# Kernel tuning notes

Hardware: AMD Instinct MI355X
Metric: run time of the kernel (lower is better)

Reference implementation:

```python
import jax, jax.numpy as jnp
import numpy as np

N_NODES = 100000
N_EDGES = 1600000
D_IN = 128
D_OUT = 256


def setup_inputs() -> dict:
    key = jax.random.key(0)
    k1, k2, k3 = jax.random.split(key, 3)
    H = jax.random.normal(k1, (N_NODES, D_IN), dtype=jnp.float32)
    edge_index = jax.random.randint(k2, (2, N_EDGES), 0, N_NODES, dtype=jnp.int64)
    # kaiming_normal_ on (in, out): fan computed over dim 1 -> std = sqrt(2/out)
    W = jax.random.normal(k3, (D_IN, D_OUT), dtype=jnp.float32) * np.sqrt(2.0 / D_OUT)
    return {"H": H, "edge_index": edge_index, "W": W}


def reference(H, edge_index, W):
    src, dst = edge_index[0], edge_index[1]
    # gather source node features per edge, scatter-add into destination nodes
    msgs = H[src]  # [E, D_IN]
    new_H = jax.ops.segment_sum(msgs, dst, num_segments=H.shape[0])  # [N, D_IN]
    out = H + new_H
    out = out @ W  # [N, D_OUT]
    return jax.nn.relu(out)
```

## Files before the change

kernel.cpp:

```cpp
#include <hip/hip_runtime.h>

#define N_NODES 100000
#define N_EDGES 1600000
#define D_IN    128
#define D_OUT   256
#define NB_SCAN ((N_NODES + 255) / 256)
#define BLK_ROWS 64
#define N_TILES  ((N_NODES + BLK_ROWS - 1) / BLK_ROWS)
#define X_ROWS   (N_TILES * BLK_ROWS)

#define NBUCK      98
#define BCAP       20480
#define BIN_CHUNK  1024
#define BIN_BLOCKS ((N_EDGES + BIN_CHUNK - 1) / BIN_CHUNK)

#define GBLK_ROWS  32
#define G_TILES    ((N_NODES + GBLK_ROWS - 1) / GBLK_ROWS)

typedef __attribute__((ext_vector_type(8))) short short8v;
typedef __attribute__((ext_vector_type(4))) float f32x4;

__device__ __forceinline__ unsigned bf16_rn(float f) {
    unsigned u = __float_as_uint(f);
    return (u + 0x7FFFu + ((u >> 16) & 1u)) >> 16;
}
__device__ __forceinline__ unsigned pack2_bf16(float a, float b) {
    return bf16_rn(a) | (bf16_rn(b) << 16);
}

__global__ void detect_idx64_kernel(const int* __restrict__ edge32,
                                    int* __restrict__ flag) {
    if (threadIdx.x == 0 && blockIdx.x == 0) {
        int is64 = 1;
        for (int i = 1; i < 32; i += 2) {
            if (edge32[i] != 0) { is64 = 0; break; }
        }
        *flag = is64;
    }
}

__device__ __forceinline__ int load_dst(const void* edge_raw, int is64, int e) {
    if (is64) return (int)((const long long*)edge_raw)[(long long)N_EDGES + e];
    return ((const int*)edge_raw)[N_EDGES + e];
}
__device__ __forceinline__ int load_src(const void* edge_raw, int is64, int e) {
    if (is64) return (int)((const long long*)edge_raw)[e];
    return ((const int*)edge_raw)[e];
}

__global__ __launch_bounds__(256) void cvt_h_kernel(
        const float* __restrict__ H, unsigned* __restrict__ Hb) {
    int i = blockIdx.x * 256 + threadIdx.x;
    if (i >= N_NODES * (D_IN / 2)) return;
    const float2 h = ((const float2*)H)[i];
    Hb[i] = pack2_bf16(h.x, h.y);
}

__global__ __launch_bounds__(256) void pack_w_kernel(
        const float* __restrict__ W, unsigned short* __restrict__ Wp) {
    int t = blockIdx.x * 256 + threadIdx.x;
    if (t >= 64 * 64) return;
    const int f  = t >> 6;
    const int l  = t & 63;
    const int nb = f >> 2;
    const int ks = f & 3;
    const int col  = nb * 16 + (l & 15);
    const int krow = ks * 32 + (l >> 4) * 8;
    #pragma unroll
    for (int i = 0; i < 8; ++i)
        Wp[(size_t)t * 8 + i] = (unsigned short)bf16_rn(W[(krow + i) * D_OUT + col]);
}

__global__ __launch_bounds__(256) void bin_hist_kernel(
        const void* __restrict__ edge_raw, const int* __restrict__ flag,
        int* __restrict__ bucket_alloc, int* __restrict__ binned) {
    __shared__ int cnt[128];
    __shared__ int gbase[128];
    const int tid = threadIdx.x;
    if (tid < 128) cnt[tid] = 0;
    __syncthreads();
    const int is64 = *flag;
    const int base = blockIdx.x * BIN_CHUNK + tid;

#define EDGE_A(i)                                                             \
    int rec##i = 0, pb##i = -1;                                               \
    {                                                                         \
        const int idx = base + (i) * 256;                                     \
        if (idx < N_EDGES) {                                                  \
            const int s = load_src(edge_raw, is64, idx);                      \
            const int d = load_dst(edge_raw, is64, idx);                      \
            if ((unsigned)s < N_NODES && (unsigned)d < N_NODES) {             \
                const int b = d >> 10;                                        \
                const int pos = atomicAdd(&cnt[b], 1);                        \
                rec##i = s | ((d & 1023) << 17);                              \
                pb##i  = pos | (b << 12);                                     \
            }                                                                 \
        }                                                                     \
    }
    EDGE_A(0) EDGE_A(1) EDGE_A(2) EDGE_A(3)
#undef EDGE_A

    __syncthreads();
    if (tid < NBUCK) gbase[tid] = atomicAdd(&bucket_alloc[tid], cnt[tid]);
    __syncthreads();

#define EDGE_B(i)                                                             \
    if (pb##i >= 0) {                                                         \
        const int b = pb##i >> 12;                                            \
        const int p = gbase[b] + (pb##i & 4095);                              \
        if (p < BCAP) binned[b * BCAP + p] = rec##i;                          \
    }
    EDGE_B(0) EDGE_B(1) EDGE_B(2) EDGE_B(3)
#undef EDGE_B
}

__global__ __launch_bounds__(512) void bucket_count_kernel(
        const int* __restrict__ bucket_alloc, const int* __restrict__ binned,
        int* __restrict__ counts) {
    __shared__ int hist[1024];
    const int b   = blockIdx.x;
    const int tid = threadIdx.x;
    for (int j = tid; j < 1024; j += 512) hist[j] = 0;
    __syncthreads();
    int cnt = bucket_alloc[b];
    if (cnt > BCAP) cnt = BCAP;
    for (int p = tid; p < cnt; p += 512) {
        const int rec = binned[b * BCAP + p];
        atomicAdd(&hist[(rec >> 17) & 1023], 1);
    }
    __syncthreads();
    const int n0 = b << 10;
    for (int j = tid; j < 1024; j += 512) {
        const int node = n0 + j;
        if (node < N_NODES) counts[node] = hist[j];
    }
}

__global__ __launch_bounds__(512) void bucket_fill_kernel(
        const int* __restrict__ row_start, const int* __restrict__ bucket_alloc,
        const int* __restrict__ binned, int* __restrict__ csr_pack) {
    __shared__ int cursor[1024];
    const int b   = blockIdx.x;
    const int tid = threadIdx.x;
    const int n0  = b << 10;
    for (int j = tid; j < 1024; j += 512) {
        const int node = n0 + j;
        cursor[j] = (node < N_NODES) ? row_start[node] : 0;
    }
    __syncthreads();
    int cnt = bucket_alloc[b];
    if (cnt > BCAP) cnt = BCAP;
    for (int p = tid; p < cnt; p += 512) {
        const int rec = binned[b * BCAP + p];
        const int dlo = (rec >> 17) & 1023;
        const int src = rec & 0x1FFFF;
        const int pos = atomicAdd(&cursor[dlo], 1);
        csr_pack[pos] = src | ((dlo & 63) << 20);
    }
}

__global__ __launch_bounds__(256) void hist_kernel(
        const void* __restrict__ edge_raw, const int* __restrict__ flag,
        int* __restrict__ counts) {
    int e = blockIdx.x * blockDim.x + threadIdx.x;
    if (e >= N_EDGES) return;
    int dst = load_dst(edge_raw, *flag, e);
    if ((unsigned)dst < N_NODES) atomicAdd(&counts[dst], 1);
}

__global__ __launch_bounds__(256) void block_sum_kernel(
        const int* __restrict__ counts, int* __restrict__ bsum) {
    __shared__ int lds[256];
    int t = threadIdx.x;
    int i = blockIdx.x * 256 + t;
    lds[t] = (i < N_NODES) ? counts[i] : 0;
    __syncthreads();
    for (int off = 128; off > 0; off >>= 1) {
        if (t < off) lds[t] += lds[t + off];
        __syncthreads();
    }
    if (t == 0) bsum[blockIdx.x] = lds[0];
}

__global__ __launch_bounds__(512) void scan_bsum_kernel(
        int* __restrict__ bsum, int* __restrict__ row_start) {
    __shared__ int lds[512];
    int t = threadIdx.x;
    lds[t] = (t < NB_SCAN) ? bsum[t] : 0;
    __syncthreads();
    for (int off = 1; off < 512; off <<= 1) {
        int u = (t >= off) ? lds[t - off] : 0;
        __syncthreads();
        lds[t] += u;
        __syncthreads();
    }
    int excl = (t == 0) ? 0 : lds[t - 1];
    if (t < NB_SCAN) bsum[t] = excl;
    if (t == 0) row_start[N_NODES] = N_EDGES;
}

__global__ __launch_bounds__(256) void scan_counts_kernel(
        int* __restrict__ counts_cursor, const int* __restrict__ bsum,
        int* __restrict__ row_start) {
    __shared__ int lds[256];
    int t = threadIdx.x;
    int i = blockIdx.x * 256 + t;
    int c = (i < N_NODES) ? counts_cursor[i] : 0;
    lds[t] = c;
    __syncthreads();
    for (int off = 1; off < 256; off <<= 1) {
        int u = (t >= off) ? lds[t - off] : 0;
        __syncthreads();
        lds[t] += u;
        __syncthreads();
    }
    int rs = bsum[blockIdx.x] + lds[t] - c;
    if (i < N_NODES) {
        row_start[i] = rs;
        counts_cursor[i] = rs;
    }
}

__global__ __launch_bounds__(256) void fill_kernel(
        const void* __restrict__ edge_raw, const int* __restrict__ flag,
        int* __restrict__ cursor, int* __restrict__ csr_pack) {
    int e = blockIdx.x * blockDim.x + threadIdx.x;
    if (e >= N_EDGES) return;
    int is64 = *flag;
    int src = load_src(edge_raw, is64, e);
    int dst = load_dst(edge_raw, is64, e);
    if ((unsigned)dst >= N_NODES || (unsigned)src >= N_NODES) return;
    int pos = atomicAdd(&cursor[dst], 1);
    csr_pack[pos] = src | ((dst & 63) << 20);
}

__global__ __launch_bounds__(256) void gather_bf16_kernel(
        const float* __restrict__ H,
        const unsigned* __restrict__ Hb,
        const int* __restrict__ row_start,
        const int* __restrict__ csr_pack,
        unsigned* __restrict__ Xg) {
    __shared__ int idx_lds[4][256];

    const int gb   = blockIdx.x * GBLK_ROWS;
    const int tile = (gb >> 6) << 6;
    const int wv   = threadIdx.x >> 6;
    const int lane = threadIdx.x & 63;
    const int r0   = gb + wv * 8;
    if (r0 >= N_NODES) return;
    int r1 = r0 + 8; if (r1 > N_NODES) r1 = N_NODES;

    const int p0   = row_start[r0];
    const int pend = row_start[r1];

    for (int r = r0; r < r1; ++r) {
        if (row_start[r + 1] == row_start[r]) {
            const float2 h = ((const float2*)(H + (size_t)r * D_IN))[lane];
            Xg[(size_t)r * 64 + lane] = pack2_bf16(h.x, h.y);
        }
    }

    int    cur = -1;
    float2 acc = make_float2(0.f, 0.f);
    float2 hs  = make_float2(0.f, 0.f);

#define FLUSH() \
    Xg[(size_t)(tile + cur) * 64 + lane] = pack2_bf16(acc.x + hs.x, acc.y + hs.y);

#define PROC(EV, UU)                                                          \
    {                                                                         \
        const int dl = (EV) >> 20;                                            \
        const float vx = __uint_as_float((UU) << 16);                         \
        const float vy = __uint_as_float((UU) & 0xFFFF0000u);                 \
        if (dl != cur) {                                                      \
            if (cur >= 0) { FLUSH(); }                                        \
            cur = dl;                                                         \
            hs  = ((const float2*)(H + (size_t)(tile + dl) * D_IN))[lane];    \
            acc = make_float2(vx, vy);                                        \
        } else {                                                              \
            acc.x += vx; acc.y += vy;                                         \
        }                                                                     \
    }

    for (int p = p0; p < pend; p += 256) {
        int m = pend - p;
        if (m > 256) m = 256;
        #pragma unroll
        for (int j = 0; j < 4; ++j) {
            const int o = lane + j * 64;
            if (o < m) idx_lds[wv][o] = csr_pack[p + o];
        }
        int n = 0;
        for (; n + 8 <= m; n += 8) {
            const int e0 = idx_lds[wv][n + 0];
            const int e1 = idx_lds[wv][n + 1];
            const int e2 = idx_lds[wv][n + 2];
            const int e3 = idx_lds[wv][n + 3];
            const int e4 = idx_lds[wv][n + 4];
            const int e5 = idx_lds[wv][n + 5];
            const int e6 = idx_lds[wv][n + 6];
            const int e7 = idx_lds[wv][n + 7];
            const unsigned u0 = Hb[(size_t)(e0 & 0xFFFFF) * 64 + lane];
            const unsigned u1 = Hb[(size_t)(e1 & 0xFFFFF) * 64 + lane];
            const unsigned u2 = Hb[(size_t)(e2 & 0xFFFFF) * 64 + lane];
            const unsigned u3 = Hb[(size_t)(e3 & 0xFFFFF) * 64 + lane];
            const unsigned u4 = Hb[(size_t)(e4 & 0xFFFFF) * 64 + lane];
            const unsigned u5 = Hb[(size_t)(e5 & 0xFFFFF) * 64 + lane];
            const unsigned u6 = Hb[(size_t)(e6 & 0xFFFFF) * 64 + lane];
            const unsigned u7 = Hb[(size_t)(e7 & 0xFFFFF) * 64 + lane];
            PROC(e0, u0) PROC(e1, u1) PROC(e2, u2) PROC(e3, u3)
            PROC(e4, u4) PROC(e5, u5) PROC(e6, u6) PROC(e7, u7)
        }
        for (; n < m; ++n) {
            const int e0 = idx_lds[wv][n];
            const unsigned u = Hb[(size_t)(e0 & 0xFFFFF) * 64 + lane];
            PROC(e0, u)
        }
    }
    if (cur >= 0) { FLUSH(); }
#undef PROC
#undef FLUSH
}

__global__ __launch_bounds__(256) void gather_f32_kernel(
        const float* __restrict__ H,
        const int* __restrict__ row_start,
        const int* __restrict__ csr_pack,
        unsigned* __restrict__ Xg) {
    __shared__ int idx_lds[4][256];

    const int gb   = blockIdx.x * GBLK_ROWS;
    const int tile = (gb >> 6) << 6;
    const int wv   = threadIdx.x >> 6;
    const int lane = threadIdx.x & 63;
    const int r0   = gb + wv * 8;
    if (r0 >= N_NODES) return;
    int r1 = r0 + 8; if (r1 > N_NODES) r1 = N_NODES;

    const int p0   = row_start[r0];
    const int pend = row_start[r1];

    for (int r = r0; r < r1; ++r) {
        if (row_start[r + 1] == row_start[r]) {
            const float2 h = ((const float2*)(H + (size_t)r * D_IN))[lane];
            Xg[(size_t)r * 64 + lane] = pack2_bf16(h.x, h.y);
        }
    }

    int    cur = -1;
    float2 acc = make_float2(0.f, 0.f);
    float2 hs  = make_float2(0.f, 0.f);

#define FLUSH() \
    Xg[(size_t)(tile + cur) * 64 + lane] = pack2_bf16(acc.x + hs.x, acc.y + hs.y);

#define PROC(EV, VV)                                                          \
    {                                                                         \
        const int dl = (EV) >> 20;                                            \
        if (dl != cur) {                                                      \
            if (cur >= 0) { FLUSH(); }                                        \
            cur = dl;                                                         \
            hs  = ((const float2*)(H + (size_t)(tile + dl) * D_IN))[lane];    \
            acc = (VV);                                                       \
        } else {                                                              \
            acc.x += (VV).x; acc.y += (VV).y;                                 \
        }                                                                     \
    }

    for (int p = p0; p < pend; p += 256) {
        int m = pend - p;
        if (m > 256) m = 256;
        #pragma unroll
        for (int j = 0; j < 4; ++j) {
            const int o = lane + j * 64;
            if (o < m) idx_lds[wv][o] = csr_pack[p + o];
        }
        int n = 0;
        for (; n + 8 <= m; n += 8) {
            const int e0 = idx_lds[wv][n + 0];
            const int e1 = idx_lds[wv][n + 1];
            const int e2 = idx_lds[wv][n + 2];
            const int e3 = idx_lds[wv][n + 3];
            const int e4 = idx_lds[wv][n + 4];
            const int e5 = idx_lds[wv][n + 5];
            const int e6 = idx_lds[wv][n + 6];
            const int e7 = idx_lds[wv][n + 7];
            const float2 v0 = ((const float2*)(H + (size_t)(e0 & 0xFFFFF) * D_IN))[lane];
            const float2 v1 = ((const float2*)(H + (size_t)(e1 & 0xFFFFF) * D_IN))[lane];
            const float2 v2 = ((const float2*)(H + (size_t)(e2 & 0xFFFFF) * D_IN))[lane];
            const float2 v3 = ((const float2*)(H + (size_t)(e3 & 0xFFFFF) * D_IN))[lane];
            const float2 v4 = ((const float2*)(H + (size_t)(e4 & 0xFFFFF) * D_IN))[lane];
            const float2 v5 = ((const float2*)(H + (size_t)(e5 & 0xFFFFF) * D_IN))[lane];
            const float2 v6 = ((const float2*)(H + (size_t)(e6 & 0xFFFFF) * D_IN))[lane];
            const float2 v7 = ((const float2*)(H + (size_t)(e7 & 0xFFFFF) * D_IN))[lane];
            PROC(e0, v0) PROC(e1, v1) PROC(e2, v2) PROC(e3, v3)
            PROC(e4, v4) PROC(e5, v5) PROC(e6, v6) PROC(e7, v7)
        }
        for (; n < m; ++n) {
            const int e0 = idx_lds[wv][n];
            const float2 v = ((const float2*)(H + (size_t)(e0 & 0xFFFFF) * D_IN))[lane];
            PROC(e0, v)
        }
    }
    if (cur >= 0) { FLUSH(); }
#undef PROC
#undef FLUSH
}

__global__ __launch_bounds__(256) void gemm_mfma_kernel(
        const unsigned* __restrict__ Xg,
        const unsigned short* __restrict__ Wp,
        float* __restrict__ out) {
    __shared__ unsigned Xs[64 * 64];

    const int tid = threadIdx.x;
    const int w   = tid >> 6;
    const int l   = tid & 63;
    const int g   = blockIdx.x * BLK_ROWS;

    #pragma unroll
    for (int j = 0; j < 4; ++j) {
        const int flat = j * 256 + tid;
        const int r   = flat >> 4;
        const int c16 = flat & 15;
        const uint4 v = *(const uint4*)(Xg + (size_t)(g + r) * 64 + c16 * 4);
        const int pc = c16 ^ (r & 7);
        *(uint4*)(&Xs[r * 64 + pc * 4]) = v;
    }

    short8v bfr[4][4];
    #pragma unroll
    for (int nb = 0; nb < 4; ++nb)
        #pragma unroll
        for (int ks = 0; ks < 4; ++ks) {
            const int f = (w * 4 + nb) * 4 + ks;
            bfr[nb][ks] = *(const short8v*)(Wp + ((size_t)f * 64 + l) * 8);
        }

    __syncthreads();

    f32x4 acc[4][4] = {};
    const int arow = l & 15;
    const int agrp = l >> 4;

    #pragma unroll
    for (int ks = 0; ks < 4; ++ks) {
        short8v a0, a1, a2, a3;
        {
            const int r = 0 * 16 + arow;
            a0 = *(const short8v*)(&Xs[r * 64 + ((ks * 4 + agrp) ^ (r & 7)) * 4]);
        }
        {
            const int r = 1 * 16 + arow;
            a1 = *(const short8v*)(&Xs[r * 64 + ((ks * 4 + agrp) ^ (r & 7)) * 4]);
        }
        {
            const int r = 2 * 16 + arow;
            a2 = *(const short8v*)(&Xs[r * 64 + ((ks * 4 + agrp) ^ (r & 7)) * 4]);
        }
        {
            const int r = 3 * 16 + arow;
            a3 = *(const short8v*)(&Xs[r * 64 + ((ks * 4 + agrp) ^ (r & 7)) * 4]);
        }
        #pragma unroll
        for (int nb = 0; nb < 4; ++nb) {
            acc[0][nb] = __builtin_amdgcn_mfma_f32_16x16x32_bf16(a0, bfr[nb][ks], acc[0][nb], 0, 0, 0);
            acc[1][nb] = __builtin_amdgcn_mfma_f32_16x16x32_bf16(a1, bfr[nb][ks], acc[1][nb], 0, 0, 0);
            acc[2][nb] = __builtin_amdgcn_mfma_f32_16x16x32_bf16(a2, bfr[nb][ks], acc[2][nb], 0, 0, 0);
            acc[3][nb] = __builtin_amdgcn_mfma_f32_16x16x32_bf16(a3, bfr[nb][ks], acc[3][nb], 0, 0, 0);
        }
    }

    #pragma unroll
    for (int mg = 0; mg < 4; ++mg) {
        #pragma unroll
        for (int rr = 0; rr < 4; ++rr) {
            const int row = g + mg * 16 + agrp * 4 + rr;
            if (row < N_NODES) {
                #pragma unroll
                for (int nb = 0; nb < 4; ++nb) {
                    const float v = acc[mg][nb][rr];
                    out[(size_t)row * D_OUT + w * 64 + nb * 16 + (l & 15)] =
                        fmaxf(v, 0.f);
                }
            }
        }
    }
}

__global__ __launch_bounds__(256) void fused_gather_gemm_relu_kernel(
        const float* __restrict__ H,
        const int* __restrict__ row_start,
        const int* __restrict__ csr_pack,
        const float* __restrict__ Wm,
        float* __restrict__ out) {
    __shared__ float Xs[BLK_ROWS][D_IN];
    __shared__ int idx_lds[4][64];

    const int g    = blockIdx.x * BLK_ROWS;
    const int tid  = threadIdx.x;
    const int wv   = tid >> 6;
    const int lane = tid & 63;

    {
        const int kidx = tid & 31;
        const int rg   = tid >> 5;
        #pragma unroll
        for (int j = 0; j < 8; ++j) {
            const int r = rg + j * 8;
            const int row = g + r;
            float4 x = make_float4(0.f, 0.f, 0.f, 0.f);
            if (row < N_NODES)
                x = *reinterpret_cast<const float4*>(H + (size_t)row * D_IN + kidx * 4);
            *reinterpret_cast<float4*>(&Xs[r][kidx * 4]) = x;
        }
    }
    __syncthreads();

    {
        const int seg_beg = row_start[g];
        const int rend    = (g + BLK_ROWS < N_NODES) ? (g + BLK_ROWS) : N_NODES;
        const int seg_end = row_start[rend];
        const int len     = seg_end - seg_beg;
        const int clen    = (len + 3) >> 2;
        const int cbeg    = seg_beg + wv * clen;
        int cend          = cbeg + clen;
        if (cend > seg_end) cend = seg_end;

        const int c2 = lane * 2;
        int   cur = -1;
        float2 acc = make_float2(0.f, 0.f);

#define PROCF(EV, VV)                                                         \
        {                                                                     \
            const int dl = (EV) >> 20;                                        \
            if (dl != cur) {                                                  \
                if (cur >= 0) {                                               \
                    atomicAdd(&Xs[cur][c2],     acc.x);                       \
                    atomicAdd(&Xs[cur][c2 + 1], acc.y);                       \
                }                                                             \
                cur = dl;                                                     \
                acc = (VV);                                                   \
            } else {                                                          \
                acc.x += (VV).x; acc.y += (VV).y;                             \
            }                                                                 \
        }

        for (int base = cbeg; base < cend; base += 64) {
            int m = cend - base;
            if (m > 64) m = 64;
            if (lane < m) idx_lds[wv][lane] = csr_pack[base + lane];
            int n = 0;
            for (; n + 8 <= m; n += 8) {
                const int e0 = idx_lds[wv][n + 0];
                const int e1 = idx_lds[wv][n + 1];
                const int e2 = idx_lds[wv][n + 2];
                const int e3 = idx_lds[wv][n + 3];
                const int e4 = idx_lds[wv][n + 4];
                const int e5 = idx_lds[wv][n + 5];
                const int e6 = idx_lds[wv][n + 6];
                const int e7 = idx_lds[wv][n + 7];
                const float2 v0 = ((const float2*)(H + (size_t)(e0 & 0xFFFFF) * D_IN))[lane];
                const float2 v1 = ((const float2*)(H + (size_t)(e1 & 0xFFFFF) * D_IN))[lane];
                const float2 v2 = ((const float2*)(H + (size_t)(e2 & 0xFFFFF) * D_IN))[lane];
                const float2 v3 = ((const float2*)(H + (size_t)(e3 & 0xFFFFF) * D_IN))[lane];
                const float2 v4 = ((const float2*)(H + (size_t)(e4 & 0xFFFFF) * D_IN))[lane];
                const float2 v5 = ((const float2*)(H + (size_t)(e5 & 0xFFFFF) * D_IN))[lane];
                const float2 v6 = ((const float2*)(H + (size_t)(e6 & 0xFFFFF) * D_IN))[lane];
                const float2 v7 = ((const float2*)(H + (size_t)(e7 & 0xFFFFF) * D_IN))[lane];
                PROCF(e0, v0) PROCF(e1, v1) PROCF(e2, v2) PROCF(e3, v3)
                PROCF(e4, v4) PROCF(e5, v5) PROCF(e6, v6) PROCF(e7, v7)
            }
            for (; n < m; ++n) {
                const int e0 = idx_lds[wv][n];
                const float2 v = ((const float2*)(H + (size_t)(e0 & 0xFFFFF) * D_IN))[lane];
                PROCF(e0, v)
            }
        }
        if (cur >= 0) {
            atomicAdd(&Xs[cur][c2],     acc.x);
            atomicAdd(&Xs[cur][c2 + 1], acc.y);
        }
#undef PROCF
    }
    __syncthreads();

    const int ty = tid >> 6;
    const int tx = tid & 63;

    float accv[16][4];
    #pragma unroll
    for (int r = 0; r < 16; ++r)
        #pragma unroll
        for (int j = 0; j < 4; ++j) accv[r][j] = 0.f;

    const float* Wp2 = Wm + tx * 4;

    #pragma unroll 2
    for (int k = 0; k < D_IN; k += 4) {
        const float4 w0 = *reinterpret_cast<const float4*>(Wp2 + (k + 0) * D_OUT);
        const float4 w1 = *reinterpret_cast<const float4*>(Wp2 + (k + 1) * D_OUT);
        const float4 w2 = *reinterpret_cast<const float4*>(Wp2 + (k + 2) * D_OUT);
        const float4 w3 = *reinterpret_cast<const float4*>(Wp2 + (k + 3) * D_OUT);
        #pragma unroll
        for (int r = 0; r < 16; ++r) {
            const float4 x = *reinterpret_cast<const float4*>(&Xs[ty * 16 + r][k]);
            accv[r][0] = fmaf(x.x, w0.x, accv[r][0]);
            accv[r][0] = fmaf(x.y, w1.x, accv[r][0]);
            accv[r][0] = fmaf(x.z, w2.x, accv[r][0]);
            accv[r][0] = fmaf(x.w, w3.x, accv[r][0]);
            accv[r][1] = fmaf(x.x, w0.y, accv[r][1]);
            accv[r][1] = fmaf(x.y, w1.y, accv[r][1]);
            accv[r][1] = fmaf(x.z, w2.y, accv[r][1]);
            accv[r][1] = fmaf(x.w, w3.y, accv[r][1]);
            accv[r][2] = fmaf(x.x, w0.z, accv[r][2]);
            accv[r][2] = fmaf(x.y, w1.z, accv[r][2]);
            accv[r][2] = fmaf(x.z, w2.z, accv[r][2]);
            accv[r][2] = fmaf(x.w, w3.z, accv[r][2]);
            accv[r][3] = fmaf(x.x, w0.w, accv[r][3]);
            accv[r][3] = fmaf(x.y, w1.w, accv[r][3]);
            accv[r][3] = fmaf(x.z, w2.w, accv[r][3]);
            accv[r][3] = fmaf(x.w, w3.w, accv[r][3]);
        }
    }

    #pragma unroll
    for (int r = 0; r < 16; ++r) {
        const int row = g + ty * 16 + r;
        if (row < N_NODES) {
            float4 o;
            o.x = fmaxf(accv[r][0], 0.f);
            o.y = fmaxf(accv[r][1], 0.f);
            o.z = fmaxf(accv[r][2], 0.f);
            o.w = fmaxf(accv[r][3], 0.f);
            *reinterpret_cast<float4*>(out + (size_t)row * D_OUT + tx * 4) = o;
        }
    }
}

extern "C" void kernel_launch(void* const* d_in, const int* in_sizes, int n_in,
                              void* d_out, int out_size, void* d_ws, size_t ws_size,
                              hipStream_t stream) {
    const float* H    = (const float*)d_in[0];
    const void*  edge = d_in[1];
    const float* Wm   = (const float*)d_in[2];
    float* out = (float*)d_out;

    const size_t off_rs    = 0;
    const size_t off_cur   = ((size_t)(N_NODES + 1) * 4 + 15) & ~(size_t)15;
    const size_t off_alloc = off_cur + (size_t)N_NODES * 4;
    const size_t off_csr   = off_alloc + 512;
    const size_t off_bsum  = off_csr + (size_t)N_EDGES * 4;
    const size_t off_flag  = off_bsum + (((size_t)NB_SCAN * 4 + 15) & ~(size_t)15);
    const size_t off_wp    = (off_flag + 16 + 255) & ~(size_t)255;
    const size_t off_X     = (off_wp + 64 * 64 * 16 + 255) & ~(size_t)255;
    const size_t need_mid  = off_X + (size_t)X_ROWS * 64 * sizeof(unsigned);
    const size_t off_Hb    = (need_mid + 255) & ~(size_t)255;
    const size_t need_full = off_Hb + (size_t)N_NODES * (D_IN / 2) * sizeof(unsigned);
    const size_t off_bin   = (need_full + 255) & ~(size_t)255;
    const size_t need_sort = off_bin + (size_t)NBUCK * BCAP * 4;

    int* row_start = (int*)((char*)d_ws + off_rs);
    int* cursor    = (int*)((char*)d_ws + off_cur);
    int* balloc    = (int*)((char*)d_ws + off_alloc);
    int* csr_pack  = (int*)((char*)d_ws + off_csr);
    int* bsum      = (int*)((char*)d_ws + off_bsum);
    int* flag      = (int*)((char*)d_ws + off_flag);
    unsigned short* Wp = (unsigned short*)((char*)d_ws + off_wp);
    unsigned* Xg   = (unsigned*)((char*)d_ws + off_X);
    unsigned* Hb   = (unsigned*)((char*)d_ws + off_Hb);
    int* binned    = (int*)((char*)d_ws + off_bin);

    detect_idx64_kernel<<<1, 64, 0, stream>>>((const int*)edge, flag);

    const int edge_blocks = (N_EDGES + 255) / 256;

    if (ws_size >= need_mid) {
        pack_w_kernel<<<16, 256, 0, stream>>>(Wm, Wp);
    }
    if (ws_size >= need_full) {
        cvt_h_kernel<<<(N_NODES * (D_IN / 2) + 255) / 256, 256, 0, stream>>>(H, Hb);
    }

    if (ws_size >= need_sort) {
        hipMemsetAsync(balloc, 0, 512, stream);
        bin_hist_kernel<<<BIN_BLOCKS, 256, 0, stream>>>(edge, flag, balloc, binned);
        bucket_count_kernel<<<NBUCK, 512, 0, stream>>>(balloc, binned, cursor);
        block_sum_kernel<<<NB_SCAN, 256, 0, stream>>>(cursor, bsum);
        scan_bsum_kernel<<<1, 512, 0, stream>>>(bsum, row_start);
        scan_counts_kernel<<<NB_SCAN, 256, 0, stream>>>(cursor, bsum, row_start);
        bucket_fill_kernel<<<NBUCK, 512, 0, stream>>>(row_start, balloc, binned, csr_pack);
    } else {
        hipMemsetAsync(cursor, 0, (size_t)N_NODES * 4 + 512, stream);
        hist_kernel<<<edge_blocks, 256, 0, stream>>>(edge, flag, cursor);
        block_sum_kernel<<<NB_SCAN, 256, 0, stream>>>(cursor, bsum);
        scan_bsum_kernel<<<1, 512, 0, stream>>>(bsum, row_start);
        scan_counts_kernel<<<NB_SCAN, 256, 0, stream>>>(cursor, bsum, row_start);
        fill_kernel<<<edge_blocks, 256, 0, stream>>>(edge, flag, cursor, csr_pack);
    }

    if (ws_size >= need_full) {
        gather_bf16_kernel<<<G_TILES, 256, 0, stream>>>(H, Hb, row_start, csr_pack, Xg);
        gemm_mfma_kernel<<<N_TILES, 256, 0, stream>>>(Xg, Wp, out);
    } else if (ws_size >= need_mid) {
        gather_f32_kernel<<<G_TILES, 256, 0, stream>>>(H, row_start, csr_pack, Xg);
        gemm_mfma_kernel<<<N_TILES, 256, 0, stream>>>(Xg, Wp, out);
    } else {
        fused_gather_gemm_relu_kernel<<<N_TILES, 256, 0, stream>>>(
            H, row_start, csr_pack, Wm, out);
    }
}
```

Baseline: 198.7 us.

## Fuse per-bucket count, scan and fill into one kernel with bucket-base scan

Replaces the bucket_count, three-kernel global prefix scan and bucket_fill sequence with a tiny 98-entry scan over bucket totals plus one kernel per bucket. That kernel builds the local histogram, scans it in LDS to produce row_start and then scatters the CSR entries. This removes several launches and the global counts round-trip. Gather-kernel stores to Xg become nontemporal. Risk: if a bucket overflows BCAP, the bucket totals no longer match the truncated counts. The serial 1024-wide LDS scan per block also adds sync overhead.

```diff
diff --git a/kernel.cpp b/kernel.cpp
--- a/kernel.cpp
+++ b/kernel.cpp
@@ -114,48 +114,58 @@
 #undef EDGE_B
 }
 
-__global__ __launch_bounds__(512) void bucket_count_kernel(
-        const int* __restrict__ bucket_alloc, const int* __restrict__ binned,
-        int* __restrict__ counts) {
+__global__ __launch_bounds__(128) void scan98_kernel(
+        const int* __restrict__ bucket_alloc, int* __restrict__ segbase) {
+    __shared__ int lds[128];
+    const int t = threadIdx.x;
+    lds[t] = (t < NBUCK) ? bucket_alloc[t] : 0;
+    __syncthreads();
+    for (int off = 1; off < 128; off <<= 1) {
+        int u = (t >= off) ? lds[t - off] : 0;
+        __syncthreads();
+        lds[t] += u;
+        __syncthreads();
+    }
+    if (t < NBUCK) segbase[t] = lds[t] - ((t < NBUCK) ? bucket_alloc[t] : 0);
+}
+
+__global__ __launch_bounds__(1024) void bucket_fill_scan_kernel(
+        const int* __restrict__ bucket_alloc, const int* __restrict__ segbase,
+        const int* __restrict__ binned,
+        int* __restrict__ row_start, int* __restrict__ csr_pack) {
     __shared__ int hist[1024];
     const int b   = blockIdx.x;
     const int tid = threadIdx.x;
-    for (int j = tid; j < 1024; j += 512) hist[j] = 0;
-    __syncthreads();
+    hist[tid] = 0;
+    __syncthreads();
+
     int cnt = bucket_alloc[b];
     if (cnt > BCAP) cnt = BCAP;
-    for (int p = tid; p < cnt; p += 512) {
-        const int rec = binned[b * BCAP + p];
-        atomicAdd(&hist[(rec >> 17) & 1023], 1);
-    }
-    __syncthreads();
-    const int n0 = b << 10;
-    for (int j = tid; j < 1024; j += 512) {
-        const int node = n0 + j;
-        if (node < N_NODES) counts[node] = hist[j];
-    }
-}
-
-__global__ __launch_bounds__(512) void bucket_fill_kernel(
-        const int* __restrict__ row_start, const int* __restrict__ bucket_alloc,
-        const int* __restrict__ binned, int* __restrict__ csr_pack) {
-    __shared__ int cursor[1024];
-    const int b   = blockIdx.x;
-    const int tid = threadIdx.x;
-    const int n0  = b << 10;
-    for (int j = tid; j < 1024; j += 512) {
-        const int node = n0 + j;
-        cursor[j] = (node < N_NODES) ? row_start[node] : 0;
-    }
-    __syncthreads();
-    int cnt = bucket_alloc[b];
-    if (cnt > BCAP) cnt = BCAP;
-    for (int p = tid; p < cnt; p += 512) {
-        const int rec = binned[b * BCAP + p];
+    const int base = b * BCAP;
+
+    for (int p = tid; p < cnt; p += 1024)
+        atomicAdd(&hist[(binned[base + p] >> 17) & 1023], 1);
+    __syncthreads();
+
+    const int myc = hist[tid];
+    for (int off = 1; off < 1024; off <<= 1) {
+        int u = (tid >= off) ? hist[tid - off] : 0;
+        __syncthreads();
+        hist[tid] += u;
+        __syncthreads();
+    }
+    const int rs = segbase[b] + hist[tid] - myc;
+    const int node = (b << 10) + tid;
+    if (node <= N_NODES) row_start[node] = rs;
+
+    hist[tid] = rs;
+    __syncthreads();
+
+    for (int p = tid; p < cnt; p += 1024) {
+        const int rec = binned[base + p];
         const int dlo = (rec >> 17) & 1023;
-        const int src = rec & 0x1FFFF;
-        const int pos = atomicAdd(&cursor[dlo], 1);
-        csr_pack[pos] = src | ((dlo & 63) << 20);
+        const int pos = atomicAdd(&hist[dlo], 1);
+        csr_pack[pos] = (rec & 0x1FFFF) | ((dlo & 63) << 20);
     }
 }
 
@@ -256,7 +266,8 @@
     for (int r = r0; r < r1; ++r) {
         if (row_start[r + 1] == row_start[r]) {
             const float2 h = ((const float2*)(H + (size_t)r * D_IN))[lane];
-            Xg[(size_t)r * 64 + lane] = pack2_bf16(h.x, h.y);
+            __builtin_nontemporal_store(pack2_bf16(h.x, h.y),
+                                        &Xg[(size_t)r * 64 + lane]);
         }
     }
 
@@ -264,8 +275,9 @@
     float2 acc = make_float2(0.f, 0.f);
     float2 hs  = make_float2(0.f, 0.f);
 
-#define FLUSH() \
-    Xg[(size_t)(tile + cur) * 64 + lane] = pack2_bf16(acc.x + hs.x, acc.y + hs.y);
+#define FLUSH()                                                               \
+    __builtin_nontemporal_store(pack2_bf16(acc.x + hs.x, acc.y + hs.y),       \
+                                &Xg[(size_t)(tile + cur) * 64 + lane]);
 
 #define PROC(EV, UU)                                                          \
     {                                                                         \
@@ -685,11 +697,9 @@
     if (ws_size >= need_sort) {
         hipMemsetAsync(balloc, 0, 512, stream);
         bin_hist_kernel<<<BIN_BLOCKS, 256, 0, stream>>>(edge, flag, balloc, binned);
-        bucket_count_kernel<<<NBUCK, 512, 0, stream>>>(balloc, binned, cursor);
-        block_sum_kernel<<<NB_SCAN, 256, 0, stream>>>(cursor, bsum);
-        scan_bsum_kernel<<<1, 512, 0, stream>>>(bsum, row_start);
-        scan_counts_kernel<<<NB_SCAN, 256, 0, stream>>>(cursor, bsum, row_start);
-        bucket_fill_kernel<<<NBUCK, 512, 0, stream>>>(row_start, balloc, binned, csr_pack);
+        scan98_kernel<<<1, 128, 0, stream>>>(balloc, bsum);
+        bucket_fill_scan_kernel<<<NBUCK, 1024, 0, stream>>>(
+            balloc, bsum, binned, row_start, csr_pack);
     } else {
         hipMemsetAsync(cursor, 0, (size_t)N_NODES * 4 + 512, stream);
         hist_kernel<<<edge_blocks, 256, 0, stream>>>(edge, flag, cursor);
```

Result: faster. 190.8 us (-3.9%).
